# Performance work log

Measured on AMD Instinct MI355X. Metric: run time of the kernel, lower is better.

Reference implementation:

```python
import jax, jax.numpy as jnp
import numpy as np

L = 3      # gat_layer_num
H = 4      # multi_num (attention heads)
N = 26     # nodes (keypoints)
F = 26     # features per node
B = 16384  # batch


def setup_inputs() -> dict:
    key = jax.random.key(0)
    ks = jax.random.split(key, 8)
    s = 1.0 / np.sqrt(F)
    x = jax.random.normal(ks[0], (B, N, F), dtype=jnp.float32)
    W = jax.random.normal(ks[1], (L, H, F, F), dtype=jnp.float32) * s
    a_src = jax.random.normal(ks[2], (L, H, F), dtype=jnp.float32) * s
    a_dst = jax.random.normal(ks[3], (L, H, F), dtype=jnp.float32) * s
    W1 = jax.random.normal(ks[4], (N * F, 256), dtype=jnp.float32) * (1.0 / np.sqrt(N * F))
    b1 = jnp.zeros((256,), dtype=jnp.float32)
    W2 = jax.random.normal(ks[5], (256, 3), dtype=jnp.float32) * (1.0 / np.sqrt(256))
    b2 = jnp.zeros((3,), dtype=jnp.float32)
    return {"dummy": 0, "x": x, "W": W, "a_src": a_src, "a_dst": a_dst,
            "W1": W1, "b1": b1, "W2": W2, "b2": b2}


def _gat_layer(x, W_l, a_src_l, a_dst_l):
    # x: [B,N,F]; W_l: [H,F,F]; a_*: [H,F]
    h = jnp.einsum('bnf,hfo->bhno', x, W_l)          # [B,H,N,F]
    s_src = jnp.einsum('bhnf,hf->bhn', h, a_src_l)    # [B,H,N]
    s_dst = jnp.einsum('bhnf,hf->bhn', h, a_dst_l)    # [B,H,N]
    e = s_src[..., :, None] + s_dst[..., None, :]     # [B,H,N,N]
    e = jax.nn.leaky_relu(e, negative_slope=0.2)
    alpha = jax.nn.softmax(e, axis=-1)                # softmax over neighbors j
    out = jnp.einsum('bhij,bhjf->bhif', alpha, h)     # [B,H,N,F]
    out = out.mean(axis=1)                            # average heads -> [B,N,F]
    return jax.nn.elu(out)


def reference(dummy, x, W, a_src, a_dst, W1, b1, W2, b2):
    for l in range(L):
        x = _gat_layer(x, W[l], a_src[l], a_dst[l])
    flat = x.reshape(x.shape[0], -1)                  # [B, N*F]
    hdn = jax.nn.leaky_relu(flat @ W1 + b1, negative_slope=0.2)
    return hdn @ W2 + b2                              # [B, 3]
```

## Files before the change

### kernel.cpp

```cpp
#include <hip/hip_runtime.h>

typedef __attribute__((ext_vector_type(8))) short s16x8;
typedef __attribute__((ext_vector_type(4))) float f32x4;
typedef unsigned short u16;
typedef unsigned int   u32;

#define MFMA16(a,b,c) __builtin_amdgcn_mfma_f32_16x16x32_bf16((a),(b),(c),0,0,0)

__device__ __forceinline__ float bf2f(u16 u){
  u32 x = ((u32)u) << 16; float f; __builtin_memcpy(&f, &x, 4); return f;
}
__device__ __forceinline__ u16 f2bf(float f){
  u32 x; __builtin_memcpy(&x, &f, 4);
  x += 0x7FFFu + ((x >> 16) & 1u);
  return (u16)(x >> 16);
}
#if defined(__has_builtin) && __has_builtin(__builtin_amdgcn_cvt_pk_bf16_f32)
__device__ __forceinline__ u32 pack2(float a, float b){
  return __builtin_bit_cast(u32, __builtin_amdgcn_cvt_pk_bf16_f32(a, b));
}
#else
__device__ __forceinline__ u32 pack2(float a, float b){
  return (u32)f2bf(a) | ((u32)f2bf(b) << 16);
}
#endif
#if defined(__has_builtin) && __has_builtin(__builtin_amdgcn_exp2f)
__device__ __forceinline__ float fexp2(float x){ return __builtin_amdgcn_exp2f(x); }
#else
extern "C" __device__ float __ocml_native_exp2_f32(float);
__device__ __forceinline__ float fexp2(float x){ return __ocml_native_exp2_f32(x); }
#endif


__global__ __launch_bounds__(256) void wprep_kernel(
    const float* __restrict__ W, const float* __restrict__ a_src,
    const float* __restrict__ a_dst, u16* __restrict__ wp)
{
  const int lh = blockIdx.x;
  const float* Wlh = W + lh*676;
  u16* dst = wp + lh*32*40;
  const int t = threadIdx.x;
  for (int e = t; e < 1280; e += 256) dst[e] = 0;
  __syncthreads();
  for (int e = t; e < 676; e += 256){ int f = e/26, o = e%26; dst[o*40 + f] = f2bf(Wlh[f*26 + o]); }
  if (t < 52){
    int sel = t/26, f = t%26;
    const float* av = (sel ? a_dst : a_src) + lh*26;
    float acc = 0.f;
    #pragma unroll
    for (int o = 0; o < 26; ++o) acc += Wlh[f*26 + o]*av[o];
    dst[(26 + sel)*40 + f] = f2bf(acc);
  }
}

__global__ __launch_bounds__(256, 4) void gat_kernel(
    const float* __restrict__ x, const u16* __restrict__ wp,
    u16* __restrict__ xf)
{
  __shared__ u16 xs [112*40];
  __shared__ u16 hsT[4*32*108 + 16];

  const int tid  = threadIdx.x;
  const int w    = tid >> 6;
  const int lane = tid & 63;
  const int q    = lane >> 4;
  const int lm   = lane & 15;
  const int b0   = blockIdx.x * 4;
  const float L2E = 1.4426950408889634f;

  for (int e = tid; e < 1728; e += 256){
    int r = e/108, c = e%108; int h = r>>2, rr = 28 + (r&3);
    hsT[(h*32 + rr)*108 + c] = 0;
  }
  for (int e = tid; e < 448; e += 256){
    int r = e>>2, c = 104 + (e&3); int h = r/28, rr = r%28;
    hsT[(h*32 + rr)*108 + c] = 0;
  }
  if (tid < 16) hsT[4*32*108 + tid] = 0;
  for (int e = tid; e < 112*14; e += 256){ int r = e/14, c = 26 + e%14; xs[r*40 + c] = 0; }
  for (int e = tid; e < 8*26;  e += 256){ int r = 104 + e/26, c = e%26; xs[r*40 + c] = 0; }
  for (int pp = tid; pp < 1352; pp += 256){
    int b = pp/338, r2 = pp%338, n = r2/13, p = r2%13;
    float2 v = *(const float2*)&x[(b0 + b)*676 + n*26 + 2*p];
    *(u32*)&xs[(b*26 + n)*40 + 2*p] = pack2(v.x, v.y);
  }

  for (int l = 0; l < 3; ++l){
    __syncthreads();

    {
      s16x8 bfr0 = *(const s16x8*)&wp[((l*4 + w)*32      + lm)*40 + q*8];
      s16x8 bfr1 = *(const s16x8*)&wp[((l*4 + w)*32 + 16 + lm)*40 + q*8];
      #pragma unroll
      for (int t = 0; t < 7; ++t){
        s16x8 af = *(const s16x8*)&xs[(t*16 + lm)*40 + q*8];
        f32x4 z = {0.f,0.f,0.f,0.f};
        f32x4 d0 = MFMA16(af, bfr0, z);
        f32x4 d1 = MFMA16(af, bfr1, z);
        int gr0 = t*16 + q*4;
        if (gr0 < 104){
          { uint2 uu; uu.x = pack2(d0[0], d0[1]); uu.y = pack2(d0[2], d0[3]);
            *(uint2*)&hsT[(w*32 + lm)*108 + gr0] = uu; }
          if (lm < 12){
            uint2 uu; uu.x = pack2(d1[0], d1[1]); uu.y = pack2(d1[2], d1[3]);
            *(uint2*)&hsT[(w*32 + 16 + lm)*108 + gr0] = uu; }
        }
      }
    }
    __syncthreads();

    {
      f32x4 acc00 = {0,0,0,0}, acc01 = acc00, acc10 = acc00, acc11 = acc00;
      const int j0 = q*8;
      const int w26 = w*26;
      #pragma unroll
      for (int h = 0; h < 4; ++h){
        s16x8 am0, am1;
        {
          int base = (h*32 + lm)*108 + w26 + j0;
          uint4 uu = { *(const u32*)&hsT[base],   *(const u32*)&hsT[base+2],
                       *(const u32*)&hsT[base+4], *(const u32*)&hsT[base+6] };
          am0 = __builtin_bit_cast(s16x8, uu);
          base = (h*32 + 16 + lm)*108 + w26 + j0;
          uint4 vv = { *(const u32*)&hsT[base],   *(const u32*)&hsT[base+2],
                       *(const u32*)&hsT[base+4], *(const u32*)&hsT[base+6] };
          am1 = __builtin_bit_cast(s16x8, vv);
        }
        float sd2[8];
        {
          int base = (h*32 + 27)*108 + w26 + j0;
          #pragma unroll
          for (int u = 0; u < 4; ++u){
            u32 v = *(const u32*)&hsT[base + 2*u];
            sd2[2*u]   = bf2f((u16)(v & 0xFFFFu)) * L2E;
            sd2[2*u+1] = bf2f((u16)(v >> 16))     * L2E;
          }
          #pragma unroll
          for (int jj = 0; jj < 8; ++jj)
            if (j0 + jj >= 26) sd2[jj] = -1e30f;
        }
        #pragma unroll
        for (int nt = 0; nt < 2; ++nt){
          int i = nt*16 + lm;
          float si2 = bf2f(hsT[(h*32 + 26)*108 + w26 + i]) * L2E;
          float p[8]; float loc = 0.f;
          #pragma unroll
          for (int jj = 0; jj < 8; ++jj){
            float e = si2 + sd2[jj];
            e = fmaxf(e, 0.2f*e);
            float pv = fexp2(e);
            p[jj] = pv; loc += pv;
          }
          float tot = loc;
          tot += __shfl_xor(tot, 16);
          tot += __shfl_xor(tot, 32);
          float rinv = __builtin_amdgcn_rcpf(tot);
          uint4 bu = { pack2(p[0]*rinv, p[1]*rinv), pack2(p[2]*rinv, p[3]*rinv),
                       pack2(p[4]*rinv, p[5]*rinv), pack2(p[6]*rinv, p[7]*rinv) };
          s16x8 bfrag = __builtin_bit_cast(s16x8, bu);
          if (nt == 0){ acc00 = MFMA16(am0, bfrag, acc00);
                        acc10 = MFMA16(am1, bfrag, acc10); }
          else        { acc01 = MFMA16(am0, bfrag, acc01);
                        acc11 = MFMA16(am1, bfrag, acc11); }
        }
      }
      #pragma unroll
      for (int nt = 0; nt < 2; ++nt){
        int i = nt*16 + lm;
        if (i < 26){
          int rowb = (w26 + i)*40;
          #pragma unroll
          for (int mt = 0; mt < 2; ++mt){
            f32x4 a = (mt == 0) ? (nt == 0 ? acc00 : acc01)
                                : (nt == 0 ? acc10 : acc11);
            int f0 = mt*16 + q*4;
            float v0 = a[0]*0.25f, v1 = a[1]*0.25f, v2 = a[2]*0.25f, v3 = a[3]*0.25f;
            v0 = (v0 > 0.f) ? v0 : (fexp2(v0*L2E) - 1.f);
            v1 = (v1 > 0.f) ? v1 : (fexp2(v1*L2E) - 1.f);
            v2 = (v2 > 0.f) ? v2 : (fexp2(v2*L2E) - 1.f);
            v3 = (v3 > 0.f) ? v3 : (fexp2(v3*L2E) - 1.f);
            if (f0 <= 20){
              uint2 uu; uu.x = pack2(v0, v1); uu.y = pack2(v2, v3);
              *(uint2*)&xs[rowb + f0] = uu;
            } else if (f0 == 24){
              *(u32*)&xs[rowb + 24] = pack2(v0, v1);
            }
          }
        }
      }
    }
  }
  __syncthreads();
  {
    const int mtile = b0 >> 4;
    const int lrow0 = b0 & 15;
    u16* dstb = xf + (size_t)mtile*22*64*8;
    for (int e = tid; e < 1408; e += 256){
      int chunk = e >> 4;
      int u     = e & 15;
      int kc = chunk >> 2, q16 = chunk & 3;
      int bb = u >> 2;
      int j2 = (u & 3) * 2;
      int k  = kc*32 + q16*8 + j2;
      u32 v = 0;
      if (k < 676){ int n = k/26, f = k - n*26; v = *(const u32*)&xs[(bb*26 + n)*40 + f]; }
      *(u32*)&dstb[((kc*64 + q16*16 + lrow0 + bb) << 3) + j2] = v;
    }
  }
}

__global__ __launch_bounds__(256) void w1cvt_kernel(const float* __restrict__ W1,
                                                    u16* __restrict__ w1t)
{
  const int k = blockIdx.x * 2;
  const int n = threadIdx.x;
  float v0 = 0.f, v1 = 0.f;
  if (k < 676)     v0 = W1[(size_t)k*256 + n];
  if (k + 1 < 676) v1 = W1[(size_t)(k+1)*256 + n];
  const int ntile = n >> 4, lm = n & 15;
  const int kc = k >> 5, q16 = (k >> 3) & 3, j = k & 7;
  u16* dst = w1t + ((((size_t)ntile*22 + kc)*64 + q16*16 + lm) << 3) + j;
  *(u32*)dst = pack2(v0, v1);
}

__global__ __launch_bounds__(256, 2) void mlp_kernel(
    const u16* __restrict__ xf, const u16* __restrict__ w1t,
    const float* __restrict__ b1, const float* __restrict__ w2,
    const float* __restrict__ b2, float* __restrict__ out)
{
  __shared__ float b1s[256];
  __shared__ float w2s[256*3];
  __shared__ float part[4*32*3];

  const int tid  = threadIdx.x;
  const int w    = tid >> 6;
  const int lane = tid & 63;
  const int q    = lane >> 4;
  const int lm   = lane & 15;
  const int m0   = blockIdx.x * 32;
  const int mt0  = blockIdx.x * 2;

  b1s[tid] = b1[tid];
  for (int e = tid; e < 768; e += 256) w2s[e] = w2[e];

  f32x4 acc[2][4];
  #pragma unroll
  for (int a = 0; a < 2; ++a)
    #pragma unroll
    for (int b = 0; b < 4; ++b) acc[a][b] = (f32x4){0.f,0.f,0.f,0.f};

  const u16* abase = xf  + ((size_t)mt0*22*64 + lane) * 8;
  const u16* bbase = w1t + (((size_t)w*4)*22*64 + lane) * 8;

  s16x8 af[2], bf[4], afn[2], bfn[4];
  #pragma unroll
  for (int mt = 0; mt < 2; ++mt) af[mt] = *(const s16x8*)(abase + (size_t)(mt*22)*64*8);
  #pragma unroll
  for (int nt = 0; nt < 4; ++nt) bf[nt] = *(const s16x8*)(bbase + (size_t)(nt*22)*64*8);

  #pragma unroll
  for (int kc = 0; kc < 22; ++kc){
    if (kc < 21){
      #pragma unroll
      for (int mt = 0; mt < 2; ++mt)
        afn[mt] = *(const s16x8*)(abase + (size_t)(mt*22 + kc + 1)*64*8);
      #pragma unroll
      for (int nt = 0; nt < 4; ++nt)
        bfn[nt] = *(const s16x8*)(bbase + (size_t)(nt*22 + kc + 1)*64*8);
    }
    #pragma unroll
    for (int mt = 0; mt < 2; ++mt)
      #pragma unroll
      for (int nt = 0; nt < 4; ++nt)
        acc[mt][nt] = MFMA16(af[mt], bf[nt], acc[mt][nt]);
    #pragma unroll
    for (int mt = 0; mt < 2; ++mt) af[mt] = afn[mt];
    #pragma unroll
    for (int nt = 0; nt < 4; ++nt) bf[nt] = bfn[nt];
  }

  float b1l[4], w2l[4][3];
  #pragma unroll
  for (int nt = 0; nt < 4; ++nt){
    int col = w*64 + nt*16 + lm;
    b1l[nt] = b1s[col];
    w2l[nt][0] = w2s[col*3]; w2l[nt][1] = w2s[col*3+1]; w2l[nt][2] = w2s[col*3+2];
  }
  float po[2][4][3];
  #pragma unroll
  for (int mt = 0; mt < 2; ++mt)
    #pragma unroll
    for (int r = 0; r < 4; ++r){
      float s0 = 0.f, s1 = 0.f, s2 = 0.f;
      #pragma unroll
      for (int nt = 0; nt < 4; ++nt){
        float hv = acc[mt][nt][r] + b1l[nt];
        hv = (hv >= 0.f) ? hv : 0.2f*hv;
        s0 += hv*w2l[nt][0]; s1 += hv*w2l[nt][1]; s2 += hv*w2l[nt][2];
      }
      po[mt][r][0] = s0; po[mt][r][1] = s1; po[mt][r][2] = s2;
    }
  #pragma unroll
  for (int m = 1; m < 16; m <<= 1)
    #pragma unroll
    for (int mt = 0; mt < 2; ++mt)
      #pragma unroll
      for (int r = 0; r < 4; ++r)
        #pragma unroll
        for (int kk = 0; kk < 3; ++kk)
          po[mt][r][kk] += __shfl_xor(po[mt][r][kk], m);
  if (lm == 0){
    #pragma unroll
    for (int mt = 0; mt < 2; ++mt)
      #pragma unroll
      for (int r = 0; r < 4; ++r)
        #pragma unroll
        for (int kk = 0; kk < 3; ++kk)
          part[w*96 + (mt*16 + q*4 + r)*3 + kk] = po[mt][r][kk];
  }
  __syncthreads();
  if (tid < 96){
    int row = tid/3, kk = tid - row*3;
    float o = part[row*3 + kk] + part[96 + row*3 + kk]
            + part[192 + row*3 + kk] + part[288 + row*3 + kk] + b2[kk];
    out[(m0 + row)*3 + kk] = o;
  }
}

extern "C" void kernel_launch(void* const* d_in, const int* in_sizes, int n_in,
                              void* d_out, int out_size, void* d_ws, size_t ws_size,
                              hipStream_t stream)
{
  (void)in_sizes; (void)n_in; (void)out_size; (void)ws_size;
  const float* x     = (const float*)d_in[1];
  const float* W     = (const float*)d_in[2];
  const float* a_src = (const float*)d_in[3];
  const float* a_dst = (const float*)d_in[4];
  const float* W1    = (const float*)d_in[5];
  const float* b1    = (const float*)d_in[6];
  const float* W2    = (const float*)d_in[7];
  const float* b2    = (const float*)d_in[8];
  float* out = (float*)d_out;

  u16* xfinal = (u16*)d_ws;
  u16* w1t    = xfinal + (size_t)16384*704;
  u16* wp     = w1t    + 256*704;

  hipLaunchKernelGGL(wprep_kernel, dim3(12),   dim3(256), 0, stream, W, a_src, a_dst, wp);
  hipLaunchKernelGGL(w1cvt_kernel, dim3(352),  dim3(256), 0, stream, W1, w1t);
  hipLaunchKernelGGL(gat_kernel,   dim3(4096), dim3(256), 0, stream, x, wp, xfinal);
  hipLaunchKernelGGL(mlp_kernel,   dim3(512),  dim3(256), 0, stream, xfinal, w1t, b1, W2, b2, out);
}
```

Before: 220.8 us.

## Merge prep kernels and repad GAT shared-memory layouts with baked-in softmax masking

The two weight-prep kernels are merged into a single launch, removing one kernel launch. In the GAT kernel, per-sample rows are padded to 32 with a 36-element stride, and the transposed h buffer uses 28 rows with a 132 stride. Padded destination columns now get -1e30 written during the projection, so the per-head masking loop in the softmax stage is gone, along with most of the zero-initialisation. It adds an eighth MFMA tile per layer and clamps out-of-range row reads, which risks wasted work or a change in bank-conflict behaviour.

```diff
diff --git a/kernel.cpp b/kernel.cpp
--- a/kernel.cpp
+++ b/kernel.cpp
@@ -32,24 +32,37 @@
 #endif
 
 
-__global__ __launch_bounds__(256) void wprep_kernel(
+__global__ __launch_bounds__(256) void prep_kernel(
     const float* __restrict__ W, const float* __restrict__ a_src,
-    const float* __restrict__ a_dst, u16* __restrict__ wp)
+    const float* __restrict__ a_dst, const float* __restrict__ W1,
+    u16* __restrict__ w1t, u16* __restrict__ wp)
 {
-  const int lh = blockIdx.x;
-  const float* Wlh = W + lh*676;
-  u16* dst = wp + lh*32*40;
   const int t = threadIdx.x;
-  for (int e = t; e < 1280; e += 256) dst[e] = 0;
-  __syncthreads();
-  for (int e = t; e < 676; e += 256){ int f = e/26, o = e%26; dst[o*40 + f] = f2bf(Wlh[f*26 + o]); }
-  if (t < 52){
-    int sel = t/26, f = t%26;
-    const float* av = (sel ? a_dst : a_src) + lh*26;
-    float acc = 0.f;
-    #pragma unroll
-    for (int o = 0; o < 26; ++o) acc += Wlh[f*26 + o]*av[o];
-    dst[(26 + sel)*40 + f] = f2bf(acc);
+  if (blockIdx.x < 352){
+    const int k = blockIdx.x * 2;
+    const int n = t;
+    float v0 = 0.f, v1 = 0.f;
+    if (k < 676)     v0 = W1[(size_t)k*256 + n];
+    if (k + 1 < 676) v1 = W1[(size_t)(k+1)*256 + n];
+    const int ntile = n >> 4, lm = n & 15;
+    const int kc = k >> 5, q16 = (k >> 3) & 3, j = k & 7;
+    u16* dst = w1t + ((((size_t)ntile*22 + kc)*64 + q16*16 + lm) << 3) + j;
+    *(u32*)dst = pack2(v0, v1);
+  } else {
+    const int lh = blockIdx.x - 352;
+    const float* Wlh = W + lh*676;
+    u16* dst = wp + lh*32*40;
+    for (int e = t; e < 1280; e += 256) dst[e] = 0;
+    __syncthreads();
+    for (int e = t; e < 676; e += 256){ int f = e/26, o = e%26; dst[o*40 + f] = f2bf(Wlh[f*26 + o]); }
+    if (t < 52){
+      int sel = t/26, f = t%26;
+      const float* av = (sel ? a_dst : a_src) + lh*26;
+      float acc = 0.f;
+      #pragma unroll
+      for (int o = 0; o < 26; ++o) acc += Wlh[f*26 + o]*av[o];
+      dst[(26 + sel)*40 + f] = f2bf(acc);
+    }
   }
 }
 
@@ -57,32 +70,33 @@
     const float* __restrict__ x, const u16* __restrict__ wp,
     u16* __restrict__ xf)
 {
-  __shared__ u16 xs [112*40];
-  __shared__ u16 hsT[4*32*108 + 16];
+  __shared__ __align__(16) u16 xs [128*36];
+  __shared__ __align__(16) u16 hsT[4*28*132];
 
   const int tid  = threadIdx.x;
   const int w    = tid >> 6;
   const int lane = tid & 63;
   const int q    = lane >> 4;
   const int lm   = lane & 15;
+  const int lmc  = (lm < 11) ? lm : 11;
   const int b0   = blockIdx.x * 4;
   const float L2E = 1.4426950408889634f;
 
-  for (int e = tid; e < 1728; e += 256){
-    int r = e/108, c = e%108; int h = r>>2, rr = 28 + (r&3);
-    hsT[(h*32 + rr)*108 + c] = 0;
-  }
-  for (int e = tid; e < 448; e += 256){
-    int r = e>>2, c = 104 + (e&3); int h = r/28, rr = r%28;
-    hsT[(h*32 + rr)*108 + c] = 0;
-  }
-  if (tid < 16) hsT[4*32*108 + tid] = 0;
-  for (int e = tid; e < 112*14; e += 256){ int r = e/14, c = 26 + e%14; xs[r*40 + c] = 0; }
-  for (int e = tid; e < 8*26;  e += 256){ int r = 104 + e/26, c = e%26; xs[r*40 + c] = 0; }
+  const bool pm01 = (lm == 11) && (q == 3);
+  const bool pm23 = (lm == 11) && (q >= 2);
+
+  for (int e = tid; e < 864; e += 256){
+    int b = e/216, r = e%216, n = 26 + r/36, c = r%36;
+    xs[(b*32 + n)*36 + c] = 0;
+  }
+  for (int e = tid; e < 1040; e += 256){
+    int r = e/10, c = 26 + e%10; int b = r/26, n = r%26;
+    xs[(b*32 + n)*36 + c] = 0;
+  }
   for (int pp = tid; pp < 1352; pp += 256){
     int b = pp/338, r2 = pp%338, n = r2/13, p = r2%13;
     float2 v = *(const float2*)&x[(b0 + b)*676 + n*26 + 2*p];
-    *(u32*)&xs[(b*26 + n)*40 + 2*p] = pack2(v.x, v.y);
+    *(u32*)&xs[(b*32 + n)*36 + 2*p] = pack2(v.x, v.y);
   }
 
   for (int l = 0; l < 3; ++l){
@@ -92,57 +106,58 @@
       s16x8 bfr0 = *(const s16x8*)&wp[((l*4 + w)*32      + lm)*40 + q*8];
       s16x8 bfr1 = *(const s16x8*)&wp[((l*4 + w)*32 + 16 + lm)*40 + q*8];
       #pragma unroll
-      for (int t = 0; t < 7; ++t){
-        s16x8 af = *(const s16x8*)&xs[(t*16 + lm)*40 + q*8];
+      for (int t = 0; t < 8; ++t){
+        s16x8 af = *(const s16x8*)&xs[(t*16 + lm)*36 + q*8];
         f32x4 z = {0.f,0.f,0.f,0.f};
         f32x4 d0 = MFMA16(af, bfr0, z);
         f32x4 d1 = MFMA16(af, bfr1, z);
-        int gr0 = t*16 + q*4;
-        if (gr0 < 104){
-          { uint2 uu; uu.x = pack2(d0[0], d0[1]); uu.y = pack2(d0[2], d0[3]);
-            *(uint2*)&hsT[(w*32 + lm)*108 + gr0] = uu; }
-          if (lm < 12){
-            uint2 uu; uu.x = pack2(d1[0], d1[1]); uu.y = pack2(d1[2], d1[3]);
-            *(uint2*)&hsT[(w*32 + 16 + lm)*108 + gr0] = uu; }
-        }
+        const int gr0 = t*16 + q*4;
+        if (t & 1){
+          d1[0] = pm01 ? -1e30f : d1[0];
+          d1[1] = pm01 ? -1e30f : d1[1];
+          d1[2] = pm23 ? -1e30f : d1[2];
+          d1[3] = pm23 ? -1e30f : d1[3];
+        }
+        { uint2 uu; uu.x = pack2(d0[0], d0[1]); uu.y = pack2(d0[2], d0[3]);
+          *(uint2*)&hsT[(w*28 + lm)*132 + gr0] = uu; }
+        if (lm < 12){
+          uint2 uu; uu.x = pack2(d1[0], d1[1]); uu.y = pack2(d1[2], d1[3]);
+          *(uint2*)&hsT[(w*28 + 16 + lm)*132 + gr0] = uu; }
       }
     }
     __syncthreads();
 
     {
       f32x4 acc00 = {0,0,0,0}, acc01 = acc00, acc10 = acc00, acc11 = acc00;
-      const int j0 = q*8;
-      const int w26 = w*26;
+      const int j0  = q*8;
+      const int b32 = w*32;
       #pragma unroll
       for (int h = 0; h < 4; ++h){
         s16x8 am0, am1;
         {
-          int base = (h*32 + lm)*108 + w26 + j0;
+          int base = (h*28 + lm)*132 + b32 + j0;
           uint4 uu = { *(const u32*)&hsT[base],   *(const u32*)&hsT[base+2],
                        *(const u32*)&hsT[base+4], *(const u32*)&hsT[base+6] };
           am0 = __builtin_bit_cast(s16x8, uu);
-          base = (h*32 + 16 + lm)*108 + w26 + j0;
+          base = (h*28 + 16 + lmc)*132 + b32 + j0;
           uint4 vv = { *(const u32*)&hsT[base],   *(const u32*)&hsT[base+2],
                        *(const u32*)&hsT[base+4], *(const u32*)&hsT[base+6] };
           am1 = __builtin_bit_cast(s16x8, vv);
         }
         float sd2[8];
         {
-          int base = (h*32 + 27)*108 + w26 + j0;
+          int base = (h*28 + 27)*132 + b32 + j0;
           #pragma unroll
           for (int u = 0; u < 4; ++u){
             u32 v = *(const u32*)&hsT[base + 2*u];
             sd2[2*u]   = bf2f((u16)(v & 0xFFFFu)) * L2E;
             sd2[2*u+1] = bf2f((u16)(v >> 16))     * L2E;
           }
-          #pragma unroll
-          for (int jj = 0; jj < 8; ++jj)
-            if (j0 + jj >= 26) sd2[jj] = -1e30f;
         }
         #pragma unroll
         for (int nt = 0; nt < 2; ++nt){
           int i = nt*16 + lm;
-          float si2 = bf2f(hsT[(h*32 + 26)*108 + w26 + i]) * L2E;
+          float si2 = bf2f(hsT[(h*28 + 26)*132 + b32 + i]) * L2E;
           float p[8]; float loc = 0.f;
           #pragma unroll
           for (int jj = 0; jj < 8; ++jj){
@@ -168,7 +183,7 @@
       for (int nt = 0; nt < 2; ++nt){
         int i = nt*16 + lm;
         if (i < 26){
-          int rowb = (w26 + i)*40;
+          int rowb = (w*32 + i)*36;
           #pragma unroll
           for (int mt = 0; mt < 2; ++mt){
             f32x4 a = (mt == 0) ? (nt == 0 ? acc00 : acc01)
@@ -203,24 +218,10 @@
       int j2 = (u & 3) * 2;
       int k  = kc*32 + q16*8 + j2;
       u32 v = 0;
-      if (k < 676){ int n = k/26, f = k - n*26; v = *(const u32*)&xs[(bb*26 + n)*40 + f]; }
+      if (k < 676){ int n = k/26, f = k - n*26; v = *(const u32*)&xs[(bb*32 + n)*36 + f]; }
       *(u32*)&dstb[((kc*64 + q16*16 + lrow0 + bb) << 3) + j2] = v;
     }
   }
-}
-
-__global__ __launch_bounds__(256) void w1cvt_kernel(const float* __restrict__ W1,
-                                                    u16* __restrict__ w1t)
-{
-  const int k = blockIdx.x * 2;
-  const int n = threadIdx.x;
-  float v0 = 0.f, v1 = 0.f;
-  if (k < 676)     v0 = W1[(size_t)k*256 + n];
-  if (k + 1 < 676) v1 = W1[(size_t)(k+1)*256 + n];
-  const int ntile = n >> 4, lm = n & 15;
-  const int kc = k >> 5, q16 = (k >> 3) & 3, j = k & 7;
-  u16* dst = w1t + ((((size_t)ntile*22 + kc)*64 + q16*16 + lm) << 3) + j;
-  *(u32*)dst = pack2(v0, v1);
 }
 
 __global__ __launch_bounds__(256, 2) void mlp_kernel(
@@ -346,8 +347,9 @@
   u16* w1t    = xfinal + (size_t)16384*704;
   u16* wp     = w1t    + 256*704;
 
-  hipLaunchKernelGGL(wprep_kernel, dim3(12),   dim3(256), 0, stream, W, a_src, a_dst, wp);
-  hipLaunchKernelGGL(w1cvt_kernel, dim3(352),  dim3(256), 0, stream, W1, w1t);
-  hipLaunchKernelGGL(gat_kernel,   dim3(4096), dim3(256), 0, stream, x, wp, xfinal);
-  hipLaunchKernelGGL(mlp_kernel,   dim3(512),  dim3(256), 0, stream, xfinal, w1t, b1, W2, b2, out);
-}
+  hipLaunchKernelGGL(prep_kernel, dim3(364),  dim3(256), 0, stream,
+                     W, a_src, a_dst, W1, w1t, wp);
+  hipLaunchKernelGGL(gat_kernel,  dim3(4096), dim3(256), 0, stream, x, wp, xfinal);
+  hipLaunchKernelGGL(mlp_kernel,  dim3(512),  dim3(256), 0, stream,
+                     xfinal, w1t, b1, W2, b2, out);
+}
```

Result: faster. 215.9 us (-2.2%).
